# Optimization experiments

Hardware: AMD Instinct MI355X
Metric: run time of the kernel (lower is better)

Reference implementation:

```python
import jax, jax.numpy as jnp
import numpy as np

NUM_HEADS = 16
SS_ATTN_ITER = 1
EPS = 1e-12


def _l2n(t):
    # F.normalize(t, dim=-1): divide by max(||t||, eps)
    return t / jnp.maximum(jnp.linalg.norm(t, axis=-1, keepdims=True), EPS)


def _self_attn(xs, inv_temp):
    # softmax(xs @ xs^T * inv_temp) @ xs, per head
    a = jax.nn.softmax(jnp.einsum('bhnd,bhmd->bhnm', xs, xs) * inv_temp, axis=-1)
    return a, jnp.einsum('bhnm,bhmd->bhnd', a, xs)


def setup_inputs() -> dict:
    key = jax.random.key(0)
    k1, k2, k3, k4 = jax.random.split(key, 4)
    N, B, C = 577, 8, 1024
    return {
        'x': jax.random.normal(k1, (N, B, C), dtype=jnp.float32),
        'qkv_w': jax.random.normal(k2, (3 * C, C), dtype=jnp.float32) * 0.02,
        'qkv_b': jax.random.normal(k3, (3 * C,), dtype=jnp.float32) * 0.02,
        'proj_w': jax.random.normal(k4, (C, C), dtype=jnp.float32) * 0.02,
        'proj_b': jnp.zeros((C,), dtype=jnp.float32),
    }


def reference(x, qkv_w, qkv_b, proj_w, proj_b):
    H = NUM_HEADS
    xb = jnp.swapaxes(x, 0, 1)  # [B, N, C]
    B, N, C = xb.shape
    hd = C // H
    scale = float(hd) ** -0.5

    qkv = (xb @ qkv_w.T + qkv_b).reshape(B, N, 3, H, hd).transpose(2, 0, 3, 1, 4)
    q, k, v = qkv[0], qkv[1], qkv[2]  # each [B, H, N, hd]

    # standard softmax attention branch
    attn_ori = jax.nn.softmax(jnp.einsum('bhnd,bhmd->bhnm', q, k) * scale, axis=-1)
    x_ori = jnp.einsum('bhnm,bhmd->bhnd', attn_ori, v).transpose(0, 2, 1, 3).reshape(B, N, C)
    x_ori = x_ori @ proj_w.T + proj_b

    # data-dependent inverse temperature (ss_attn_temp is None)
    pre_norm = jnp.linalg.norm(xb, axis=-1).mean(axis=-1)[:, None, None, None]  # [B,1,1,1]
    inv_temp = pre_norm * scale

    xs1, xs2, xs3 = v, k, q
    for _ in range(SS_ATTN_ITER):
        xs1, xs2, xs3 = _l2n(xs1), _l2n(xs2), _l2n(xs3)
        _, xs1 = _self_attn(xs1, inv_temp)
        _, xs2 = _self_attn(xs2, inv_temp)
        _, xs3 = _self_attn(xs3, inv_temp)

    xs1, xs2, xs3 = _l2n(xs1), _l2n(xs2), _l2n(xs3)
    a1, _ = _self_attn(xs1, inv_temp)
    a2, _ = _self_attn(xs2, inv_temp)
    a3, _ = _self_attn(xs3, inv_temp)
    xs = (jnp.einsum('bhnm,bhmd->bhnd', a1, v)
          + jnp.einsum('bhnm,bhmd->bhnd', a2, v)
          + jnp.einsum('bhnm,bhmd->bhnd', a3, v)) / 3.0

    x_gem = xs.transpose(0, 2, 1, 3).reshape(B, N, C) @ proj_w.T + proj_b
    return (jnp.swapaxes(x_gem, 0, 1), jnp.swapaxes(x_ori, 0, 1))
```

## Files before the change

kernel.cpp:

```cpp
#include <hip/hip_runtime.h>
#include <math.h>

#define NTOK 577
#define NB 8
#define NC 1024
#define NH 16
#define HD 64
#define M_ROWS (NB*NTOK)
#define SZ ((size_t)NB*NH*NTOK*HD)
#define WSZ ((size_t)3*NC*NC)
#define PSZ ((size_t)NC*NC)
#define VTW 608
#define VTSZ ((size_t)NB*NH*HD*VTW)
#define HSTR ((size_t)NTOK*HD)
#define LP 36
#define LOG2E 1.44269504088896f

typedef __attribute__((ext_vector_type(8)))  short bf16x8_t;
typedef __attribute__((ext_vector_type(8)))  unsigned short u16x8_t;
typedef __attribute__((ext_vector_type(16))) float f32x16_t;

union U4 { unsigned short s[8]; unsigned int u[4]; bf16x8_t v; };

__device__ inline unsigned short f2bf(float x){
    unsigned int u = __float_as_uint(x);
    u = (u + 0x7FFFu + ((u>>16)&1u)) >> 16;
    return (unsigned short)u;
}
__device__ inline float bf2f(unsigned short h){
    return __uint_as_float(((unsigned int)h)<<16);
}
__device__ inline unsigned int cvt_pk(float a, float b){
    unsigned int r;
    asm volatile("v_cvt_pk_bf16_f32 %0, %1, %2" : "=v"(r) : "v"(a), "v"(b));
    return r;
}
__device__ inline float fexp2(float x){
    float r;
    asm("v_exp_f32 %0, %1" : "=v"(r) : "v"(x));
    return r;
}

__global__ __launch_bounds__(256) void split_all(const float* __restrict__ X,
        const float* __restrict__ W, const float* __restrict__ P,
        unsigned short* __restrict__ xh, unsigned short* __restrict__ xl,
        unsigned short* __restrict__ wh, unsigned short* __restrict__ ph,
        float* __restrict__ rn)
{
    int row = blockIdx.x, t = threadIdx.x;
    if (row < M_ROWS){
        int b = row / NTOK, n = row % NTOK;
        const float* s = X + ((size_t)n*NB + b)*NC + 4*t;
        float4 v = *(const float4*)s;
        ushort4 hv, lv;
        hv.x = f2bf(v.x); lv.x = f2bf(v.x - bf2f(hv.x));
        hv.y = f2bf(v.y); lv.y = f2bf(v.y - bf2f(hv.y));
        hv.z = f2bf(v.z); lv.z = f2bf(v.z - bf2f(hv.z));
        hv.w = f2bf(v.w); lv.w = f2bf(v.w - bf2f(hv.w));
        *(ushort4*)(xh + (size_t)row*NC + 4*t) = hv;
        *(ushort4*)(xl + (size_t)row*NC + 4*t) = lv;
        float ss = v.x*v.x + v.y*v.y + v.z*v.z + v.w*v.w;
        #pragma unroll
        for (int o = 1; o < 64; o <<= 1) ss += __shfl_xor(ss, o);
        __shared__ float red[4];
        if ((t & 63) == 0) red[t >> 6] = ss;
        __syncthreads();
        if (t == 0) rn[row] = sqrtf(red[0] + red[1] + red[2] + red[3]);
    } else if (row < M_ROWS + 3*NC){
        size_t drow = row - M_ROWS;
        float4 v = *(const float4*)(W + drow*NC + 4*t);
        ushort4 hv;
        hv.x = f2bf(v.x); hv.y = f2bf(v.y); hv.z = f2bf(v.z); hv.w = f2bf(v.w);
        *(ushort4*)(wh + drow*NC + 4*t) = hv;
    } else {
        size_t drow = row - M_ROWS - 3*NC;
        float4 v = *(const float4*)(P + drow*NC + 4*t);
        ushort4 hv;
        hv.x = f2bf(v.x); hv.y = f2bf(v.y); hv.z = f2bf(v.z); hv.w = f2bf(v.w);
        *(ushort4*)(ph + drow*NC + 4*t) = hv;
    }
}

__global__ __launch_bounds__(256) void calc_invtemp(const float* __restrict__ rn,
                                                    float* __restrict__ it)
{
    int b = blockIdx.x;
    int tid = threadIdx.x;
    float s = 0.f;
    for (int i = tid; i < NTOK; i += 256) s += rn[b*NTOK + i];
    #pragma unroll
    for (int o = 1; o < 64; o <<= 1) s += __shfl_xor(s, o);
    __shared__ float red[4];
    if ((tid & 63) == 0) red[tid >> 6] = s;
    __syncthreads();
    if (tid == 0) it[b] = (red[0]+red[1]+red[2]+red[3]) / (float)NTOK * 0.125f;
}

__device__ __forceinline__ void transp_body(const unsigned short* src,
                                            unsigned short* dst)
{
    __shared__ unsigned short t[64][72];
    int bh = blockIdx.y;
    int n0 = blockIdx.x * 64;
    int tid = threadIdx.x;
    int r  = tid >> 2;
    int c0 = (tid & 3) * 16;
    int n = n0 + r;
    if (n < NTOK){
        const unsigned short* s = src + ((size_t)bh*NTOK + n)*HD + c0;
        *(u16x8_t*)&t[r][c0]   = *(const u16x8_t*)s;
        *(u16x8_t*)&t[r][c0+8] = *(const u16x8_t*)(s + 8);
    } else {
        u16x8_t z = (u16x8_t)0;
        *(u16x8_t*)&t[r][c0]   = z;
        *(u16x8_t*)&t[r][c0+8] = z;
    }
    __syncthreads();
    if (n0 + c0 < VTW){
        int d = r;
        U4 o0, o1;
        #pragma unroll
        for (int j = 0; j < 8; j++){ o0.s[j] = t[c0+j][d]; o1.s[j] = t[c0+8+j][d]; }
        unsigned short* dp = dst + ((size_t)bh*HD + d)*VTW + n0 + c0;
        *(u16x8_t*)dp       = (u16x8_t)o0.v;
        *(u16x8_t*)(dp + 8) = (u16x8_t)o1.v;
    }
}

__global__ __launch_bounds__(256) void transp64(const unsigned short* __restrict__ src,
                                                unsigned short* __restrict__ dst)
{
    transp_body(src, dst);
}

__global__ __launch_bounds__(256) void transp64x3(
    const unsigned short* __restrict__ s0, unsigned short* __restrict__ d0,
    const unsigned short* __restrict__ s1, unsigned short* __restrict__ d1,
    const unsigned short* __restrict__ s2, unsigned short* __restrict__ d2)
{
    int i = blockIdx.z;
    const unsigned short* s = (i == 0) ? s0 : (i == 1 ? s1 : s2);
    unsigned short* d = (i == 0) ? d0 : (i == 1 ? d1 : d2);
    transp_body(s, d);
}

#define MFMA8(a0h,a1h,b0,b1,a0l,a1l) \
    acc[0][0] = __builtin_amdgcn_mfma_f32_32x32x16_bf16(a0h, b0, acc[0][0], 0,0,0); \
    acc[0][1] = __builtin_amdgcn_mfma_f32_32x32x16_bf16(a0h, b1, acc[0][1], 0,0,0); \
    acc[1][0] = __builtin_amdgcn_mfma_f32_32x32x16_bf16(a1h, b0, acc[1][0], 0,0,0); \
    acc[1][1] = __builtin_amdgcn_mfma_f32_32x32x16_bf16(a1h, b1, acc[1][1], 0,0,0); \
    acc[0][0] = __builtin_amdgcn_mfma_f32_32x32x16_bf16(a0l, b0, acc[0][0], 0,0,0); \
    acc[0][1] = __builtin_amdgcn_mfma_f32_32x32x16_bf16(a0l, b1, acc[0][1], 0,0,0); \
    acc[1][0] = __builtin_amdgcn_mfma_f32_32x32x16_bf16(a1l, b0, acc[1][0], 0,0,0); \
    acc[1][1] = __builtin_amdgcn_mfma_f32_32x32x16_bf16(a1l, b1, acc[1][1], 0,0,0);

__global__ __launch_bounds__(256) void gemm_qkv_mfma(
    const unsigned short* __restrict__ Ah, const unsigned short* __restrict__ Al,
    const unsigned short* __restrict__ Bh,
    const float* __restrict__ bias,
    unsigned short* __restrict__ qh, unsigned short* __restrict__ ql,
    unsigned short* __restrict__ kh, unsigned short* __restrict__ kl,
    unsigned short* __restrict__ vh, unsigned short* __restrict__ vl)
{
    __shared__ unsigned short ahs[128][LP], als[128][LP];
    __shared__ unsigned short bhs[128][LP];
    int t = threadIdx.x;
    int l = t & 63, w = t >> 6;
    int lq = l & 31, hi = l >> 5;
    int wr = w >> 1, wc = w & 1;
    int col0 = blockIdx.x*128, row0 = blockIdx.y*128;

    int srow[2], scol[2], sa[2];
    #pragma unroll
    for (int i = 0; i < 2; i++){
        int idx = i*256 + t;
        srow[i] = idx >> 2;
        scol[i] = (idx & 3) * 8;
        int ar = row0 + srow[i]; if (ar >= M_ROWS) ar = M_ROWS-1;
        sa[i] = ar;
    }

    f32x16_t acc[2][2];
    #pragma unroll
    for (int i = 0; i < 16; i++){
        acc[0][0][i]=0.f; acc[0][1][i]=0.f; acc[1][0][i]=0.f; acc[1][1][i]=0.f;
    }

    for (int k0 = 0; k0 < NC; k0 += 32){
        if (k0) __syncthreads();
        #pragma unroll
        for (int i = 0; i < 2; i++){
            size_t ao = (size_t)sa[i]*NC + k0 + scol[i];
            size_t bo = (size_t)(col0 + srow[i])*NC + k0 + scol[i];
            u16x8_t va  = *(const u16x8_t*)(Ah + ao);
            u16x8_t va2 = *(const u16x8_t*)(Al + ao);
            u16x8_t vb  = *(const u16x8_t*)(Bh + bo);
            *(u16x8_t*)&ahs[srow[i]][scol[i]] = va;
            *(u16x8_t*)&als[srow[i]][scol[i]] = va2;
            *(u16x8_t*)&bhs[srow[i]][scol[i]] = vb;
        }
        __syncthreads();
        #pragma unroll
        for (int kk = 0; kk < 2; kk++){
            int co = kk*16 + 8*hi;
            bf16x8_t a0h = *(const bf16x8_t*)&ahs[wr*64+lq][co];
            bf16x8_t a1h = *(const bf16x8_t*)&ahs[wr*64+32+lq][co];
            bf16x8_t b0  = *(const bf16x8_t*)&bhs[wc*64+lq][co];
            bf16x8_t b1  = *(const bf16x8_t*)&bhs[wc*64+32+lq][co];
            bf16x8_t a0l = *(const bf16x8_t*)&als[wr*64+lq][co];
            bf16x8_t a1l = *(const bf16x8_t*)&als[wr*64+32+lq][co];
            MFMA8(a0h,a1h,b0,b1,a0l,a1l)
        }
    }

    int colW = col0 + wc*64, rowW = row0 + wr*64;
    #pragma unroll
    for (int fn = 0; fn < 2; fn++){
        int colb = colW + fn*32 + lq;
        float bb = bias[colb];
        int tt = colb >> 10, h = (colb >> 6) & 15, d = colb & 63;
        unsigned short* dsth = (tt == 0) ? qh : (tt == 1 ? kh : vh);
        unsigned short* dstl = (tt == 0) ? ql : (tt == 1 ? kl : vl);
        #pragma unroll
        for (int fm = 0; fm < 2; fm++){
            #pragma unroll
            for (int r = 0; r < 16; r++){
                int orow = rowW + fm*32 + (r&3) + 8*(r>>2) + 4*hi;
                if (orow < M_ROWS){
                    float val = acc[fm][fn][r] + bb;
                    int b = orow / NTOK, n = orow % NTOK;
                    unsigned short hv = f2bf(val);
                    unsigned short lv = f2bf(val - bf2f(hv));
                    size_t idx = ((size_t)(b*NH + h)*NTOK + n)*HD + d;
                    dsth[idx] = hv; dstl[idx] = lv;
                }
            }
        }
    }
}

template<int NA>
__device__ __forceinline__ void proj_body(
    const unsigned short* A0h, const unsigned short* A0l,
    const unsigned short* A1h, const unsigned short* A1l,
    const unsigned short* A2h, const unsigned short* A2l,
    const unsigned short* Bh,
    const float* bias, float alpha, float* out, int bx, int by)
{
    __shared__ unsigned short ahs[64][LP], als[64][LP];
    __shared__ unsigned short bhs[128][LP];
    int t = threadIdx.x;
    int l = t & 63, w = t >> 6;
    int lq = l & 31, hi = l >> 5;
    int wr = w >> 1, wc = w & 1;
    int col0 = bx*128, row0 = by*64;

    int sarow = t >> 2, sacol = (t & 3) * 8;
    int ar = row0 + sarow; if (ar >= M_ROWS) ar = M_ROWS-1;
    size_t abase = (size_t)(ar / NTOK)*NH*HSTR + (size_t)(ar % NTOK)*HD;
    int sbrow[2], sbcol[2];
    #pragma unroll
    for (int i = 0; i < 2; i++){
        int idx = i*256 + t;
        sbrow[i] = idx >> 2;
        sbcol[i] = (idx & 3) * 8;
    }

    f32x16_t acc[2];
    #pragma unroll
    for (int i = 0; i < 16; i++){ acc[0][i]=0.f; acc[1][i]=0.f; }

    for (int k0 = 0; k0 < NC; k0 += 32){
        if (k0) __syncthreads();
        {
            int kk = k0 + sacol;
            size_t ao = abase + (size_t)(kk >> 6)*HSTR + (kk & 63);
            U4 h0, l0;
            u16x8_t va  = *(const u16x8_t*)(A0h + ao);
            u16x8_t va2 = *(const u16x8_t*)(A0l + ao);
            if (NA == 3){
                u16x8_t vb  = *(const u16x8_t*)(A1h + ao);
                u16x8_t vb2 = *(const u16x8_t*)(A1l + ao);
                u16x8_t vc  = *(const u16x8_t*)(A2h + ao);
                u16x8_t vc2 = *(const u16x8_t*)(A2l + ao);
                #pragma unroll
                for (int j = 0; j < 8; j++){
                    float s = bf2f(va[j]) + bf2f(va2[j]) + bf2f(vb[j])
                            + bf2f(vb2[j]) + bf2f(vc[j]) + bf2f(vc2[j]);
                    unsigned short hv = f2bf(s);
                    h0.s[j] = hv; l0.s[j] = f2bf(s - bf2f(hv));
                }
                *(u16x8_t*)&ahs[sarow][sacol] = (u16x8_t)h0.v;
                *(u16x8_t*)&als[sarow][sacol] = (u16x8_t)l0.v;
            } else {
                *(u16x8_t*)&ahs[sarow][sacol] = va;
                *(u16x8_t*)&als[sarow][sacol] = va2;
            }
            #pragma unroll
            for (int i = 0; i < 2; i++){
                size_t bo = (size_t)(col0 + sbrow[i])*NC + k0 + sbcol[i];
                u16x8_t vb = *(const u16x8_t*)(Bh + bo);
                *(u16x8_t*)&bhs[sbrow[i]][sbcol[i]] = vb;
            }
        }
        __syncthreads();
        #pragma unroll
        for (int kk = 0; kk < 2; kk++){
            int co = kk*16 + 8*hi;
            bf16x8_t a0h = *(const bf16x8_t*)&ahs[wr*32+lq][co];
            bf16x8_t a0l = *(const bf16x8_t*)&als[wr*32+lq][co];
            bf16x8_t b0  = *(const bf16x8_t*)&bhs[wc*64+lq][co];
            bf16x8_t b1  = *(const bf16x8_t*)&bhs[wc*64+32+lq][co];
            acc[0] = __builtin_amdgcn_mfma_f32_32x32x16_bf16(a0h, b0, acc[0], 0,0,0);
            acc[1] = __builtin_amdgcn_mfma_f32_32x32x16_bf16(a0h, b1, acc[1], 0,0,0);
            acc[0] = __builtin_amdgcn_mfma_f32_32x32x16_bf16(a0l, b0, acc[0], 0,0,0);
            acc[1] = __builtin_amdgcn_mfma_f32_32x32x16_bf16(a0l, b1, acc[1], 0,0,0);
        }
    }

    #pragma unroll
    for (int fn = 0; fn < 2; fn++){
        int colb = col0 + wc*64 + fn*32 + lq;
        float bb = bias[colb];
        #pragma unroll
        for (int r = 0; r < 16; r++){
            int orow = row0 + wr*32 + (r&3) + 8*(r>>2) + 4*hi;
            if (orow < M_ROWS){
                int b = orow / NTOK, n = orow % NTOK;
                out[((size_t)n*NB + b)*NC + colb] = alpha*acc[fn][r] + bb;
            }
        }
    }
}

__global__ __launch_bounds__(256) void proj2(
    const unsigned short* __restrict__ A0h, const unsigned short* __restrict__ A0l,
    const unsigned short* __restrict__ A1h, const unsigned short* __restrict__ A1l,
    const unsigned short* __restrict__ A2h, const unsigned short* __restrict__ A2l,
    const unsigned short* __restrict__ Oh, const unsigned short* __restrict__ Ol,
    const unsigned short* __restrict__ Bh,
    const float* __restrict__ bias, float* __restrict__ out_gem,
    float* __restrict__ out_ori)
{
    if (blockIdx.z == 0)
        proj_body<3>(A0h,A0l,A1h,A1l,A2h,A2l,Bh,bias,1.f/3.f,out_gem,
                     blockIdx.x, blockIdx.y);
    else
        proj_body<1>(Oh,Ol,Oh,Ol,Oh,Ol,Bh,bias,1.f,out_ori,
                     blockIdx.x, blockIdx.y);
}

__device__ __forceinline__ void stage_load(
    const unsigned short* Kh, const unsigned short* VT,
    size_t base, size_t vtb, int kt, int t, u16x8_t& rk, u16x8_t& rv)
{
    int krow = t >> 3, kslot = t & 7;
    int kr = kt*32 + krow; if (kr >= NTOK) kr = NTOK-1;
    rk = *(const u16x8_t*)(Kh + base + (size_t)kr*HD + kslot*8);
    int vrow = t >> 2, vslot = t & 3;
    rv = *(const u16x8_t*)(VT + vtb + (size_t)vrow*VTW + kt*32 + vslot*8);
}

__device__ __forceinline__ void stage_write(
    unsigned short* kbuf, unsigned short* vbuf, int t,
    const u16x8_t rk, const u16x8_t rv)
{
    int krow = t >> 3, kslot = t & 7;
    int kb = krow*128 + ((kslot*16) ^ ((krow & 7) << 4));
    *(u16x8_t*)((char*)kbuf + kb) = rk;
    int vrow = t >> 2, vslot = t & 3;
    int vb = vrow*64 + ((vslot*16) ^ ((vrow & 3) << 4));
    *(u16x8_t*)((char*)vbuf + vb) = rv;
}

template<int VAR>
__device__ __forceinline__ void flash_body2(
    const unsigned short* Qh, const unsigned short* Kh,
    const unsigned short* VT,
    unsigned short* Ohi, unsigned short* Olo,
    float scale, int bh, int qt, int tid,
    unsigned short (*kbufs)[2048], unsigned short (*vbufs)[2048])
{
    int lane = tid & 63;
    int hi = lane >> 5, lq = lane & 31;
    const size_t base = (size_t)bh * NTOK * HD;
    const size_t vtb  = (size_t)bh * HD * VTW;
    const float l2s = scale * LOG2E;

    int qrow = qt*32 + lq;
    int qr = qrow < NTOK ? qrow : NTOK-1;
    const size_t qoff = base + (size_t)qr*HD + 8*hi;
    bf16x8_t qfh[4];
    #pragma unroll
    for (int c = 0; c < 4; c++)
        qfh[c] = *(const bf16x8_t*)(Qh + qoff + 16*c);

    f32x16_t od0, od1;
    #pragma unroll
    for (int r = 0; r < 16; r++){ od0[r]=0.f; od1[r]=0.f; }
    float m_ = -1e30f, l_ = 0.f;

    u16x8_t rk, rv;
    stage_load(Kh, VT, base, vtb, 0, tid, rk, rv);
    stage_write(kbufs[0], vbufs[0], tid, rk, rv);
    __syncthreads();
    int cur = 0;

    for (int kt = 0; kt < 19; kt++){
        if (kt < 18) stage_load(Kh, VT, base, vtb, kt+1, tid, rk, rv);

        const char* kb = (const char*)kbufs[cur];
        const char* vb = (const char*)vbufs[cur];
        bf16x8_t kfh[4];
        #pragma unroll
        for (int c = 0; c < 4; c++)
            kfh[c] = *(const bf16x8_t*)(kb + lq*128 +
                        ((32*c + 16*hi) ^ ((lq & 7) << 4)));
        f32x16_t sf;
        #pragma unroll
        for (int r = 0; r < 16; r++) sf[r] = 0.f;
        __builtin_amdgcn_s_setprio(1);
        #pragma unroll
        for (int c = 0; c < 4; c++)
            sf = __builtin_amdgcn_mfma_f32_32x32x16_bf16(kfh[c], qfh[c], sf, 0,0,0);
        __builtin_amdgcn_s_setprio(0);

        float p[16];
        if (VAR == 0){
            float tm = -1e30f;
            if (kt == 18){
                #pragma unroll
                for (int r = 0; r < 16; r++){
                    int key = 576 + (r&3) + 8*(r>>2) + 4*hi;
                    p[r] = (key < NTOK) ? sf[r]*l2s : -1e30f;
                    tm = fmaxf(tm, p[r]);
                }
            } else {
                #pragma unroll
                for (int r = 0; r < 16; r++){ p[r] = sf[r]*l2s; tm = fmaxf(tm, p[r]); }
            }
            tm = fmaxf(tm, __shfl_xor(tm, 32));
            float mn = fmaxf(m_, tm);
            float corr = fexp2(m_ - mn);
            float ps = 0.f;
            #pragma unroll
            for (int r = 0; r < 16; r++){ p[r] = fexp2(p[r] - mn); ps += p[r]; }
            ps += __shfl_xor(ps, 32);
            l_ = l_*corr + ps;
            m_ = mn;
            #pragma unroll
            for (int r = 0; r < 16; r++){
                int crow = (r&3) + 8*(r>>2) + 4*hi;
                float cR = __shfl(corr, crow);
                od0[r] *= cR; od1[r] *= cR;
            }
        } else {
            if (kt == 18){
                #pragma unroll
                for (int r = 0; r < 16; r++){
                    int key = 576 + (r&3) + 8*(r>>2) + 4*hi;
                    p[r] = (key < NTOK) ? fexp2(sf[r]*l2s - l2s) : 0.f;
                }
            } else {
                #pragma unroll
                for (int r = 0; r < 16; r++) p[r] = fexp2(sf[r]*l2s - l2s);
            }
            if (VAR == 2){
                #pragma unroll
                for (int r = 0; r < 16; r++) l_ += p[r];
            }
        }

        U4 pa[2];
        #pragma unroll
        for (int ks = 0; ks < 2; ks++){
            unsigned int X0 = cvt_pk(p[8*ks+0], p[8*ks+1]);
            unsigned int X1 = cvt_pk(p[8*ks+2], p[8*ks+3]);
            unsigned int X2 = cvt_pk(p[8*ks+4], p[8*ks+5]);
            unsigned int X3 = cvt_pk(p[8*ks+6], p[8*ks+7]);
            unsigned int Y0 = (unsigned int)__shfl_xor((int)X2, 32);
            unsigned int Y1 = (unsigned int)__shfl_xor((int)X3, 32);
            unsigned int Y2 = (unsigned int)__shfl_xor((int)X0, 32);
            unsigned int Y3 = (unsigned int)__shfl_xor((int)X1, 32);
            pa[ks].u[0] = hi ? Y0 : X0;
            pa[ks].u[1] = hi ? Y1 : X1;
            pa[ks].u[2] = hi ? X2 : Y2;
            pa[ks].u[3] = hi ? X3 : Y3;
        }
        int vsw = (lq & 3) << 4;
        bf16x8_t vf00 = *(const bf16x8_t*)(vb + lq*64      + ((16*hi)      ^ vsw));
        bf16x8_t vf01 = *(const bf16x8_t*)(vb + lq*64      + ((32 + 16*hi) ^ vsw));
        bf16x8_t vf10 = *(const bf16x8_t*)(vb + (32+lq)*64 + ((16*hi)      ^ vsw));
        bf16x8_t vf11 = *(const bf16x8_t*)(vb + (32+lq)*64 + ((32 + 16*hi) ^ vsw));
        __builtin_amdgcn_s_setprio(1);
        od0 = __builtin_amdgcn_mfma_f32_32x32x16_bf16(pa[0].v, vf00, od0, 0,0,0);
        od0 = __builtin_amdgcn_mfma_f32_32x32x16_bf16(pa[1].v, vf01, od0, 0,0,0);
        od1 = __builtin_amdgcn_mfma_f32_32x32x16_bf16(pa[0].v, vf10, od1, 0,0,0);
        od1 = __builtin_amdgcn_mfma_f32_32x32x16_bf16(pa[1].v, vf11, od1, 0,0,0);
        __builtin_amdgcn_s_setprio(0);

        if (kt < 18) stage_write(kbufs[cur^1], vbufs[cur^1], tid, rk, rv);
        __syncthreads();
        cur ^= 1;
    }

    if (VAR == 1){
        #pragma unroll
        for (int r = 0; r < 16; r++){
            float s = od0[r]*od0[r] + od1[r]*od1[r];
            #pragma unroll
            for (int o = 1; o < 32; o <<= 1) s += __shfl_xor(s, o);
            int crow = (r&3) + 8*(r>>2) + 4*hi;
            int qg = qt*32 + crow;
            if (qg < NTOK){
                float inv = 1.f / fmaxf(sqrtf(s), 1e-12f);
                size_t o0 = base + (size_t)qg*HD + lq;
                Ohi[o0]    = f2bf(od0[r]*inv);
                Ohi[o0+32] = f2bf(od1[r]*inv);
            }
        }
        return;
    }

    if (VAR == 2) l_ = l_ + __shfl_xor(l_, 32);
    float linv = 1.f / l_;
    #pragma unroll
    for (int r = 0; r < 16; r++){
        int crow = (r&3) + 8*(r>>2) + 4*hi;
        int qg = qt*32 + crow;
        float li = __shfl(linv, crow);
        if (qg < NTOK){
            size_t o0 = base + (size_t)qg*HD + lq;
            float a0 = od0[r]*li, a1 = od1[r]*li;
            unsigned short h0 = f2bf(a0), h1 = f2bf(a1);
            Ohi[o0] = h0;    Olo[o0]    = f2bf(a0 - bf2f(h0));
            Ohi[o0+32] = h1; Olo[o0+32] = f2bf(a1 - bf2f(h1));
        }
    }
}

__global__ __launch_bounds__(256) void flash4(
    const unsigned short* __restrict__ x1h,
    const unsigned short* __restrict__ x2h,
    const unsigned short* __restrict__ x3h,
    const unsigned short* __restrict__ qh_,
    const unsigned short* __restrict__ kh_,
    const unsigned short* __restrict__ vt1, const unsigned short* __restrict__ vt2,
    const unsigned short* __restrict__ vt3, const unsigned short* __restrict__ vtv,
    unsigned short* __restrict__ z1h,
    unsigned short* __restrict__ z2h,
    unsigned short* __restrict__ z3h,
    unsigned short* __restrict__ ooh, unsigned short* __restrict__ ool,
    const float* __restrict__ itemp)
{
    __shared__ unsigned short kbufs[2][2048], vbufs[2][2048];
    int bid = blockIdx.x;
    int bh = (bid & 7) * 16 + (bid >> 3) / 5;
    int w = threadIdx.x >> 6;
    int qt = ((bid >> 3) % 5) * 4 + w; if (qt > 18) qt = 18;
    int i = blockIdx.y;
    if (i == 3){
        flash_body2<0>(qh_, kh_, vtv, ooh, ool, 0.125f, bh, qt,
                       threadIdx.x, kbufs, vbufs);
    } else {
        const unsigned short *Qh, *VT;
        unsigned short *Oh;
        if (i == 0){ Qh=x1h; VT=vt1; Oh=z1h; }
        else if (i == 1){ Qh=x2h; VT=vt2; Oh=z2h; }
        else { Qh=x3h; VT=vt3; Oh=z3h; }
        flash_body2<1>(Qh, Qh, VT, Oh, nullptr, itemp[bh >> 4], bh, qt,
                       threadIdx.x, kbufs, vbufs);
    }
}

__global__ __launch_bounds__(256) void flashfin(
    const unsigned short* __restrict__ z1h,
    const unsigned short* __restrict__ z2h,
    const unsigned short* __restrict__ z3h,
    const unsigned short* __restrict__ vtv,
    unsigned short* __restrict__ o0h, unsigned short* __restrict__ o0l,
    unsigned short* __restrict__ o1h, unsigned short* __restrict__ o1l,
    unsigned short* __restrict__ o2h, unsigned short* __restrict__ o2l,
    const float* __restrict__ itemp)
{
    __shared__ unsigned short kbufs[2][2048], vbufs[2][2048];
    int bid = blockIdx.x;
    int bh = (bid & 7) * 16 + (bid >> 3) / 5;
    int w = threadIdx.x >> 6;
    int qt = ((bid >> 3) % 5) * 4 + w; if (qt > 18) qt = 18;
    int i = blockIdx.y;
    const unsigned short* Qh;
    unsigned short *Oh, *Ol;
    if (i == 0){ Qh=z1h; Oh=o0h; Ol=o0l; }
    else if (i == 1){ Qh=z2h; Oh=o1h; Ol=o1l; }
    else { Qh=z3h; Oh=o2h; Ol=o2l; }
    flash_body2<2>(Qh, Qh, vtv, Oh, Ol, itemp[bh >> 4], bh, qt,
                   threadIdx.x, kbufs, vbufs);
}

__device__ __forceinline__ void l2n_body(const unsigned short* ih,
        const unsigned short* il, unsigned short* oh, unsigned short* ol)
{
    size_t row = (size_t)blockIdx.x*4 + (threadIdx.x >> 6);
    int lane = threadIdx.x & 63;
    size_t ii = row*HD + lane;
    float x = bf2f(ih[ii]) + bf2f(il[ii]);
    float s = x*x;
    #pragma unroll
    for (int o = 1; o < 64; o <<= 1) s += __shfl_xor(s, o);
    float xn = x / fmaxf(sqrtf(s), 1e-12f);
    unsigned short hv = f2bf(xn);
    oh[ii] = hv;
    ol[ii] = f2bf(xn - bf2f(hv));
}

__global__ __launch_bounds__(256) void l2n3(
    const unsigned short* __restrict__ i0h, const unsigned short* __restrict__ i0l,
    unsigned short* __restrict__ o0h, unsigned short* __restrict__ o0l,
    const unsigned short* __restrict__ i1h, const unsigned short* __restrict__ i1l,
    unsigned short* __restrict__ o1h, unsigned short* __restrict__ o1l,
    const unsigned short* __restrict__ i2h, const unsigned short* __restrict__ i2l,
    unsigned short* __restrict__ o2h, unsigned short* __restrict__ o2l)
{
    int i = blockIdx.y;
    if (i == 0) l2n_body(i0h, i0l, o0h, o0l);
    else if (i == 1) l2n_body(i1h, i1l, o1h, o1l);
    else l2n_body(i2h, i2l, o2h, o2l);
}

extern "C" void kernel_launch(void* const* d_in, const int* in_sizes, int n_in,
                              void* d_out, int out_size, void* d_ws, size_t ws_size,
                              hipStream_t stream)
{
    const float* x      = (const float*)d_in[0];
    const float* qkv_w  = (const float*)d_in[1];
    const float* qkv_b  = (const float*)d_in[2];
    const float* proj_w = (const float*)d_in[3];
    const float* proj_b = (const float*)d_in[4];
    float* out = (float*)d_out;

    unsigned short* w16 = (unsigned short*)d_ws;
    #define SL(i) (w16 + (size_t)(i)*SZ)
    unsigned short* WQh = w16 + 8*SZ;
    unsigned short* VT1 = WQh;
    size_t p = 8*SZ + 2*WSZ;
    unsigned short* VTv = w16 + p;  p += VTSZ;
    unsigned short* VT2 = w16 + p;  p += VTSZ;
    unsigned short* VT3 = w16 + p;  p += VTSZ;
    unsigned short* WPh = w16 + p;  p += PSZ;
    p += PSZ;
    unsigned short* E0  = w16 + p;  p += SZ;
    unsigned short* E1  = w16 + p;  p += SZ;
    float* rn = (float*)(w16 + p);  p += 2*(M_ROWS + 8);
    float* it = rn + M_ROWS;
    unsigned short* F0 = w16 + p;  p += SZ;
    unsigned short* F1 = w16 + p;  p += SZ;
    unsigned short* G0 = w16 + p;  p += SZ;
    p += SZ;

    dim3 blk(256);
    dim3 gq(24,37), gt(10,128), gt3(10,128,3), gl3(18464,3);
    dim3 gfl4(640,4), gfl3(640,3), gp2(8,73,2);

    split_all<<<dim3(M_ROWS + 4*NC), blk, 0, stream>>>(x, qkv_w, proj_w,
        SL(6), SL(7), WQh, WPh, rn);
    calc_invtemp<<<dim3(NB), blk, 0, stream>>>(rn, it);
    gemm_qkv_mfma<<<gq, blk, 0, stream>>>(SL(6), SL(7), WQh, qkv_b,
        SL(0), SL(1), SL(2), SL(3), SL(4), SL(5));
    transp64<<<gt, blk, 0, stream>>>(SL(4), VTv);

    l2n3<<<gl3, blk, 0, stream>>>(
        SL(4),SL(5), SL(4),SL(5),
        SL(2),SL(3), SL(6),SL(7),
        SL(0),SL(1), E0,E1);
    transp64x3<<<gt3, blk, 0, stream>>>(SL(4), VT1, SL(6), VT2, E0, VT3);

    flash4<<<gfl4, blk, 0, stream>>>(
        SL(4), SL(6), E0,
        SL(0), SL(2),
        VT1, VT2, VT3, VTv,
        F0, F1, G0, SL(1), SL(3), it);

    flashfin<<<gfl3, blk, 0, stream>>>(
        F0, F1, G0, VTv,
        SL(4),SL(5), SL(6),SL(7), E0,E1, it);

    proj2<<<gp2, blk, 0, stream>>>(
        SL(4),SL(5), SL(6),SL(7), E0,E1,
        SL(1),SL(3),
        WPh, proj_b, out, out + SZ);
    #undef SL
}
```

Baseline: 480.8 us.

## Process two key tiles per barrier and skip rescale when running max stable

Restructures the flash attention loop to stage two 32-key tiles per double-buffer slot, which halves the number of block barriers. The next pair's global loads are issued before the first tile is processed, and that first tile is written back to shared memory between the two tile computations. The standard softmax variant now skips the output rescale whenever the new tile max stays within a threshold of the running max across the wave (a lazy-rescale trick). The VT column clamp keeps the extra prefetch in bounds. LDS per block doubles and register pressure rises from holding two staged tiles, which may reduce occupancy.

```diff
diff --git a/kernel.cpp b/kernel.cpp
--- a/kernel.cpp
+++ b/kernel.cpp
@@ -358,7 +358,8 @@
     int kr = kt*32 + krow; if (kr >= NTOK) kr = NTOK-1;
     rk = *(const u16x8_t*)(Kh + base + (size_t)kr*HD + kslot*8);
     int vrow = t >> 2, vslot = t & 3;
-    rv = *(const u16x8_t*)(VT + vtb + (size_t)vrow*VTW + kt*32 + vslot*8);
+    int vc = kt*32; if (vc > VTW-32) vc = VTW-32;
+    rv = *(const u16x8_t*)(VT + vtb + (size_t)vrow*VTW + vc + vslot*8);
 }
 
 __device__ __forceinline__ void stage_write(
@@ -374,12 +375,112 @@
 }
 
 template<int VAR>
+__device__ __forceinline__ void flash_tile(
+    const unsigned short* kbuf, const unsigned short* vbuf,
+    int kt, const bf16x8_t* qfh, float l2s, int hi, int lq,
+    f32x16_t& od0, f32x16_t& od1, float& m_, float& l_)
+{
+    const char* kb = (const char*)kbuf;
+    const char* vb = (const char*)vbuf;
+    bf16x8_t kfh[4];
+    #pragma unroll
+    for (int c = 0; c < 4; c++)
+        kfh[c] = *(const bf16x8_t*)(kb + lq*128 +
+                    ((32*c + 16*hi) ^ ((lq & 7) << 4)));
+    f32x16_t sf;
+    #pragma unroll
+    for (int r = 0; r < 16; r++) sf[r] = 0.f;
+    __builtin_amdgcn_s_setprio(1);
+    #pragma unroll
+    for (int c = 0; c < 4; c++)
+        sf = __builtin_amdgcn_mfma_f32_32x32x16_bf16(kfh[c], qfh[c], sf, 0,0,0);
+    __builtin_amdgcn_s_setprio(0);
+
+    float p[16];
+    if (VAR == 0){
+        float tm = -1e30f;
+        if (kt == 18){
+            #pragma unroll
+            for (int r = 0; r < 16; r++){
+                int key = 576 + (r&3) + 8*(r>>2) + 4*hi;
+                p[r] = (key < NTOK) ? sf[r]*l2s : -1e30f;
+                tm = fmaxf(tm, p[r]);
+            }
+        } else {
+            #pragma unroll
+            for (int r = 0; r < 16; r++){ p[r] = sf[r]*l2s; tm = fmaxf(tm, p[r]); }
+        }
+        tm = fmaxf(tm, __shfl_xor(tm, 32));
+        if (!__all(tm <= m_ + 8.f)){
+            float mn = fmaxf(m_, tm);
+            float corr = fexp2(m_ - mn);
+            l_ *= corr;
+            m_ = mn;
+            #pragma unroll
+            for (int r = 0; r < 16; r++){
+                int crow = (r&3) + 8*(r>>2) + 4*hi;
+                float cR = __shfl(corr, crow);
+                od0[r] *= cR; od1[r] *= cR;
+            }
+        }
+        float ps = 0.f;
+        #pragma unroll
+        for (int r = 0; r < 16; r++){ p[r] = fexp2(p[r] - m_); ps += p[r]; }
+        ps += __shfl_xor(ps, 32);
+        l_ += ps;
+    } else {
+        if (kt == 18){
+            #pragma unroll
+            for (int r = 0; r < 16; r++){
+                int key = 576 + (r&3) + 8*(r>>2) + 4*hi;
+                p[r] = (key < NTOK) ? fexp2(sf[r]*l2s - l2s) : 0.f;
+            }
+        } else {
+            #pragma unroll
+            for (int r = 0; r < 16; r++) p[r] = fexp2(sf[r]*l2s - l2s);
+        }
+        if (VAR == 2){
+            #pragma unroll
+            for (int r = 0; r < 16; r++) l_ += p[r];
+        }
+    }
+
+    U4 pa[2];
+    #pragma unroll
+    for (int ks = 0; ks < 2; ks++){
+        unsigned int X0 = cvt_pk(p[8*ks+0], p[8*ks+1]);
+        unsigned int X1 = cvt_pk(p[8*ks+2], p[8*ks+3]);
+        unsigned int X2 = cvt_pk(p[8*ks+4], p[8*ks+5]);
+        unsigned int X3 = cvt_pk(p[8*ks+6], p[8*ks+7]);
+        unsigned int Y0 = (unsigned int)__shfl_xor((int)X2, 32);
+        unsigned int Y1 = (unsigned int)__shfl_xor((int)X3, 32);
+        unsigned int Y2 = (unsigned int)__shfl_xor((int)X0, 32);
+        unsigned int Y3 = (unsigned int)__shfl_xor((int)X1, 32);
+        pa[ks].u[0] = hi ? Y0 : X0;
+        pa[ks].u[1] = hi ? Y1 : X1;
+        pa[ks].u[2] = hi ? X2 : Y2;
+        pa[ks].u[3] = hi ? X3 : Y3;
+    }
+    int vsw = (lq & 3) << 4;
+    bf16x8_t vf00 = *(const bf16x8_t*)(vb + lq*64      + ((16*hi)      ^ vsw));
+    bf16x8_t vf01 = *(const bf16x8_t*)(vb + lq*64      + ((32 + 16*hi) ^ vsw));
+    bf16x8_t vf10 = *(const bf16x8_t*)(vb + (32+lq)*64 + ((16*hi)      ^ vsw));
+    bf16x8_t vf11 = *(const bf16x8_t*)(vb + (32+lq)*64 + ((32 + 16*hi) ^ vsw));
+    __builtin_amdgcn_s_setprio(1);
+    od0 = __builtin_amdgcn_mfma_f32_32x32x16_bf16(pa[0].v, vf00, od0, 0,0,0);
+    od0 = __builtin_amdgcn_mfma_f32_32x32x16_bf16(pa[1].v, vf01, od0, 0,0,0);
+    od1 = __builtin_amdgcn_mfma_f32_32x32x16_bf16(pa[0].v, vf10, od1, 0,0,0);
+    od1 = __builtin_amdgcn_mfma_f32_32x32x16_bf16(pa[1].v, vf11, od1, 0,0,0);
+    __builtin_amdgcn_s_setprio(0);
+}
+
+template<int VAR>
 __device__ __forceinline__ void flash_body2(
     const unsigned short* Qh, const unsigned short* Kh,
     const unsigned short* VT,
     unsigned short* Ohi, unsigned short* Olo,
     float scale, int bh, int qt, int tid,
-    unsigned short (*kbufs)[2048], unsigned short (*vbufs)[2048])
+    unsigned short (*kbufs)[2][2048], unsigned short (*vbufs)[2][2048])
 {
     int lane = tid & 63;
     int hi = lane >> 5, lq = lane & 31;
@@ -400,106 +501,29 @@
     for (int r = 0; r < 16; r++){ od0[r]=0.f; od1[r]=0.f; }
     float m_ = -1e30f, l_ = 0.f;
 
-    u16x8_t rk, rv;
-    stage_load(Kh, VT, base, vtb, 0, tid, rk, rv);
-    stage_write(kbufs[0], vbufs[0], tid, rk, rv);
+    u16x8_t rk0, rv0, rk1, rv1;
+    stage_load(Kh, VT, base, vtb, 0, tid, rk0, rv0);
+    stage_load(Kh, VT, base, vtb, 1, tid, rk1, rv1);
+    stage_write(kbufs[0][0], vbufs[0][0], tid, rk0, rv0);
+    stage_write(kbufs[0][1], vbufs[0][1], tid, rk1, rv1);
     __syncthreads();
     int cur = 0;
 
-    for (int kt = 0; kt < 19; kt++){
-        if (kt < 18) stage_load(Kh, VT, base, vtb, kt+1, tid, rk, rv);
-
-        const char* kb = (const char*)kbufs[cur];
-        const char* vb = (const char*)vbufs[cur];
-        bf16x8_t kfh[4];
-        #pragma unroll
-        for (int c = 0; c < 4; c++)
-            kfh[c] = *(const bf16x8_t*)(kb + lq*128 +
-                        ((32*c + 16*hi) ^ ((lq & 7) << 4)));
-        f32x16_t sf;
-        #pragma unroll
-        for (int r = 0; r < 16; r++) sf[r] = 0.f;
-        __builtin_amdgcn_s_setprio(1);
-        #pragma unroll
-        for (int c = 0; c < 4; c++)
-            sf = __builtin_amdgcn_mfma_f32_32x32x16_bf16(kfh[c], qfh[c], sf, 0,0,0);
-        __builtin_amdgcn_s_setprio(0);
-
-        float p[16];
-        if (VAR == 0){
-            float tm = -1e30f;
-            if (kt == 18){
-                #pragma unroll
-                for (int r = 0; r < 16; r++){
-                    int key = 576 + (r&3) + 8*(r>>2) + 4*hi;
-                    p[r] = (key < NTOK) ? sf[r]*l2s : -1e30f;
-                    tm = fmaxf(tm, p[r]);
-                }
-            } else {
-                #pragma unroll
-                for (int r = 0; r < 16; r++){ p[r] = sf[r]*l2s; tm = fmaxf(tm, p[r]); }
-            }
-            tm = fmaxf(tm, __shfl_xor(tm, 32));
-            float mn = fmaxf(m_, tm);
-            float corr = fexp2(m_ - mn);
-            float ps = 0.f;
-            #pragma unroll
-            for (int r = 0; r < 16; r++){ p[r] = fexp2(p[r] - mn); ps += p[r]; }
-            ps += __shfl_xor(ps, 32);
-            l_ = l_*corr + ps;
-            m_ = mn;
-            #pragma unroll
-            for (int r = 0; r < 16; r++){
-                int crow = (r&3) + 8*(r>>2) + 4*hi;
-                float cR = __shfl(corr, crow);
-                od0[r] *= cR; od1[r] *= cR;
-            }
-        } else {
-            if (kt == 18){
-                #pragma unroll
-                for (int r = 0; r < 16; r++){
-                    int key = 576 + (r&3) + 8*(r>>2) + 4*hi;
-                    p[r] = (key < NTOK) ? fexp2(sf[r]*l2s - l2s) : 0.f;
-                }
-            } else {
-                #pragma unroll
-                for (int r = 0; r < 16; r++) p[r] = fexp2(sf[r]*l2s - l2s);
-            }
-            if (VAR == 2){
-                #pragma unroll
-                for (int r = 0; r < 16; r++) l_ += p[r];
-            }
-        }
-
-        U4 pa[2];
-        #pragma unroll
-        for (int ks = 0; ks < 2; ks++){
-            unsigned int X0 = cvt_pk(p[8*ks+0], p[8*ks+1]);
-            unsigned int X1 = cvt_pk(p[8*ks+2], p[8*ks+3]);
-            unsigned int X2 = cvt_pk(p[8*ks+4], p[8*ks+5]);
-            unsigned int X3 = cvt_pk(p[8*ks+6], p[8*ks+7]);
-            unsigned int Y0 = (unsigned int)__shfl_xor((int)X2, 32);
-            unsigned int Y1 = (unsigned int)__shfl_xor((int)X3, 32);
-            unsigned int Y2 = (unsigned int)__shfl_xor((int)X0, 32);
-            unsigned int Y3 = (unsigned int)__shfl_xor((int)X1, 32);
-            pa[ks].u[0] = hi ? Y0 : X0;
-            pa[ks].u[1] = hi ? Y1 : X1;
-            pa[ks].u[2] = hi ? X2 : Y2;
-            pa[ks].u[3] = hi ? X3 : Y3;
-        }
-        int vsw = (lq & 3) << 4;
-        bf16x8_t vf00 = *(const bf16x8_t*)(vb + lq*64      + ((16*hi)      ^ vsw));
-        bf16x8_t vf01 = *(const bf16x8_t*)(vb + lq*64      + ((32 + 16*hi) ^ vsw));
-        bf16x8_t vf10 = *(const bf16x8_t*)(vb + (32+lq)*64 + ((16*hi)      ^ vsw));
-        bf16x8_t vf11 = *(const bf16x8_t*)(vb + (32+lq)*64 + ((32 + 16*hi) ^ vsw));
-        __builtin_amdgcn_s_setprio(1);
-        od0 = __builtin_amdgcn_mfma_f32_32x32x16_bf16(pa[0].v, vf00, od0, 0,0,0);
-        od0 = __builtin_amdgcn_mfma_f32_32x32x16_bf16(pa[1].v, vf01, od0, 0,0,0);
-        od1 = __builtin_amdgcn_mfma_f32_32x32x16_bf16(pa[0].v, vf10, od1, 0,0,0);
-        od1 = __builtin_amdgcn_mfma_f32_32x32x16_bf16(pa[1].v, vf11, od1, 0,0,0);
-        __builtin_amdgcn_s_setprio(0);
-
-        if (kt < 18) stage_write(kbufs[cur^1], vbufs[cur^1], tid, rk, rv);
+    for (int i = 0; i < 10; i++){
+        int kt0 = 2*i;
+        if (i < 9){
+            stage_load(Kh, VT, base, vtb, kt0+2, tid, rk0, rv0);
+            stage_load(Kh, VT, base, vtb, kt0+3, tid, rk1, rv1);
+        }
+        flash_tile<VAR>(kbufs[cur][0], vbufs[cur][0], kt0, qfh, l2s, hi, lq,
+                        od0, od1, m_, l_);
+        if (i < 9){
+            stage_write(kbufs[cur^1][0], vbufs[cur^1][0], tid, rk0, rv0);
+            stage_write(kbufs[cur^1][1], vbufs[cur^1][1], tid, rk1, rv1);
+        }
+        if (kt0 + 1 < 19)
+            flash_tile<VAR>(kbufs[cur][1], vbufs[cur][1], kt0+1, qfh, l2s, hi, lq,
+                            od0, od1, m_, l_);
         __syncthreads();
         cur ^= 1;
     }
@@ -553,7 +577,7 @@
     unsigned short* __restrict__ ooh, unsigned short* __restrict__ ool,
     const float* __restrict__ itemp)
 {
-    __shared__ unsigned short kbufs[2][2048], vbufs[2][2048];
+    __shared__ unsigned short kbufs[2][2][2048], vbufs[2][2][2048];
     int bid = blockIdx.x;
     int bh = (bid & 7) * 16 + (bid >> 3) / 5;
     int w = threadIdx.x >> 6;
@@ -583,7 +607,7 @@
     unsigned short* __restrict__ o2h, unsigned short* __restrict__ o2l,
     const float* __restrict__ itemp)
 {
-    __shared__ unsigned short kbufs[2][2048], vbufs[2][2048];
+    __shared__ unsigned short kbufs[2][2][2048], vbufs[2][2][2048];
     int bid = blockIdx.x;
     int bh = (bid & 7) * 16 + (bid >> 3) / 5;
     int w = threadIdx.x >> 6;
```

After: 454.4 us. -5.5%, faster.
